# Performance work log

Measured on AMD Instinct MI355X. Metric: run time of the kernel, lower is better.

Reference implementation:

```python
import jax, jax.numpy as jnp
import numpy as np

B, M, N, D = 32, 10, 1000, 128
DEMAND_SCALER, SPEED_SCALER, PREF_SCALER = 40.0, 1.0, 1.0


def _pos_encoding(m, d, dtype):
    # standard sinusoidal PE over agent positions 0..m-1
    pos = jnp.arange(m, dtype=dtype)[:, None]
    div = jnp.exp(jnp.arange(0, d, 2, dtype=dtype) * (-jnp.log(jnp.asarray(10000.0, dtype)) / d))
    ang = pos * div  # (m, d/2)
    return jnp.stack([jnp.sin(ang), jnp.cos(ang)], axis=-1).reshape(m, d)  # even=sin, odd=cos


def setup_inputs() -> dict:
    key = jax.random.key(0)
    ks = jax.random.split(key, 14)
    return {
        "locs": jax.random.uniform(ks[0], (B, M + N, 2), jnp.float32),
        "capacity": jax.random.uniform(ks[1], (B, M), jnp.float32),
        "speed": jax.random.uniform(ks[2], (B, M), jnp.float32),
        "demand": jax.random.uniform(ks[3], (B, 1, M + N), jnp.float32),
        "agents_preference": jax.random.uniform(ks[4], (B, M, M + N), jnp.float32),
        "action_mask": jnp.ones((B, M, M + N), dtype=bool),
        "W_depot": jax.random.normal(ks[5], (D, 2), jnp.float32) * 0.1,
        "W_posproj": jax.random.normal(ks[6], (D, D), jnp.float32) * 0.05,
        "alpha": jnp.ones((1,), jnp.float32),
        "W_agents": jax.random.normal(ks[7], (D, 4), jnp.float32) * 0.1,
        "W_depot_agents": jax.random.normal(ks[8], (D, 2 * D), jnp.float32) * 0.05,
        "W_clients": jax.random.normal(ks[9], (D, 5), jnp.float32) * 0.1,
        "W_pref": jax.random.normal(ks[10], (D, 1), jnp.float32) * 0.1,
        "W_final": jax.random.normal(ks[11], (D, 3 * D), jnp.float32) * 0.05,
    }


def reference(locs, capacity, speed, demand, agents_preference, action_mask,
              W_depot, W_posproj, alpha, W_agents, W_depot_agents, W_clients,
              W_pref, W_final):
    m = action_mask.shape[-2]
    d = W_final.shape[0]
    depot_locs = locs[:, :m]            # (B, m, 2)
    agents_locs = locs[:, :m]
    clients_locs = locs[:, m:]          # (B, N, 2)

    # depot branch with positional encoding
    dep_emb = depot_locs @ W_depot.T                                   # (B, m, D)
    pe = _pos_encoding(m, d, dep_emb.dtype)                            # (m, D)
    depot_embedding = dep_emb + alpha[0] * (pe @ W_posproj.T)          # broadcast over B

    # agents branch
    agents_feats = jnp.concatenate(
        [agents_locs, capacity[..., None] / DEMAND_SCALER, speed[..., None] / SPEED_SCALER], axis=-1)
    agents_embedding = agents_feats @ W_agents.T                       # (B, m, D)
    depot_agents_embedding = jnp.concatenate(
        [depot_embedding, agents_embedding], axis=-1) @ W_depot_agents.T  # (B, m, D)

    # clients branch (with polar feats)
    demands = demand[:, 0, m:]                                         # (B, N)
    centered = clients_locs - depot_locs[:, 0:1]                       # (B, N, 2)
    dist = jnp.linalg.norm(centered, axis=-1, keepdims=True)
    angle = jnp.arctan2(centered[..., 1:], centered[..., :1])
    clients_feats = jnp.concatenate(
        [clients_locs, demands[..., None] / DEMAND_SCALER, dist, angle], axis=-1)
    clients_embedding = clients_feats @ W_clients.T                    # (B, N, D)

    nodes_embedding = jnp.concatenate([agents_embedding, clients_embedding], axis=1)  # (B, m+N, D)

    # fused final projection: Linear(3D, D) on cat([nodes, pref_embed, depot_agents])
    # == nodes @ Wn.T  +  pref_embed @ Wp.T  +  depot_agents @ Wd.T, broadcast over dims.
    # pref_embed = pref[..., None] * W_pref[:, 0]  (rank-1), so pref_embed @ Wp.T = pref[..., None] * (Wp @ W_pref[:, 0])
    Wn, Wp, Wd = W_final[:, :d], W_final[:, d:2 * d], W_final[:, 2 * d:]
    v_pref = Wp @ W_pref[:, 0]                                         # (D,)
    pref = agents_preference / PREF_SCALER                             # (B, m, m+N)
    combined_embedding = (
        (nodes_embedding @ Wn.T)[:, None, :, :]                        # (B, 1, m+N, D)
        + pref[..., None] * v_pref                                     # (B, m, m+N, D)
        + (depot_agents_embedding @ Wd.T)[:, :, None, :]               # (B, m, 1, D)
    )
    return nodes_embedding, combined_embedding
```

## Files before the change

kernel.cpp:

```cpp
#include <hip/hip_runtime.h>
#include <math.h>

#define BB 32
#define MM 10
#define NNODES 1010
#define DD 128
#define RPB 32
#define NG ((NNODES + RPB - 1) / RPB)

__global__ __launch_bounds__(512) void k_agents(
    const float* __restrict__ locs,
    const float* __restrict__ capacity,
    const float* __restrict__ speed,
    const float* __restrict__ W_depot,
    const float* __restrict__ W_posproj,
    const float* __restrict__ alpha,
    const float* __restrict__ W_agents,
    const float* __restrict__ W_da,
    const float* __restrict__ W_pref,
    const float* __restrict__ W_final,
    float* __restrict__ out_nodes,
    float* __restrict__ ws_daWd,
    float* __restrict__ ws_vpref)
{
    const int b = blockIdx.x / MM;
    const int m = blockIdx.x % MM;
    const int t = threadIdx.x;
    const int d = t & (DD - 1);
    const int q = t >> 7;

    __shared__ float pe_s[DD];
    __shared__ float dep_s[DD];
    __shared__ float ag_s[DD];
    __shared__ float da_s[DD];
    __shared__ float part[4][DD];

    if (q == 0) {
        const int i = d >> 1;
        const float div = expf((float)(2 * i) * (-logf(10000.0f) / (float)DD));
        const float ang = (float)m * div;
        pe_s[d] = (d & 1) ? cosf(ang) : sinf(ang);
    }
    __syncthreads();

    float pp = 0.0f;
    {
        const float4* wp  = (const float4*)(W_posproj + (size_t)d * DD + q * 32);
        const float4* pe4 = (const float4*)(pe_s + q * 32);
        #pragma unroll
        for (int k4 = 0; k4 < 8; ++k4) {
            const float4 w = wp[k4], p = pe4[k4];
            pp = fmaf(w.x, p.x, fmaf(w.y, p.y, fmaf(w.z, p.z, fmaf(w.w, p.w, pp))));
        }
    }
    part[q][d] = pp;
    __syncthreads();

    if (q == 0) {
        const float ppf = part[0][d] + part[1][d] + part[2][d] + part[3][d];
        const float lx = locs[((size_t)b * NNODES + m) * 2 + 0];
        const float ly = locs[((size_t)b * NNODES + m) * 2 + 1];
        const float dep = fmaf(lx, W_depot[d * 2 + 0],
                          fmaf(ly, W_depot[d * 2 + 1], alpha[0] * ppf));
        const float cap = capacity[b * MM + m] * (1.0f / 40.0f);
        const float spd = speed[b * MM + m];
        const float ag = fmaf(lx, W_agents[d * 4 + 0],
                         fmaf(ly, W_agents[d * 4 + 1],
                         fmaf(cap, W_agents[d * 4 + 2],
                              spd * W_agents[d * 4 + 3])));
        out_nodes[((size_t)b * NNODES + m) * DD + d] = ag;
        dep_s[d] = dep;
        ag_s[d] = ag;
    }
    __syncthreads();

    float da = 0.0f;
    {
        const float4* s4  = (const float4*)((q < 2) ? (dep_s + q * 64)
                                                    : (ag_s + (q - 2) * 64));
        const float4* wda = (const float4*)(W_da + (size_t)d * 2 * DD + q * 64);
        #pragma unroll
        for (int k4 = 0; k4 < 16; ++k4) {
            const float4 w = wda[k4], p = s4[k4];
            da = fmaf(w.x, p.x, fmaf(w.y, p.y, fmaf(w.z, p.z, fmaf(w.w, p.w, da))));
        }
    }
    part[q][d] = da;
    __syncthreads();
    if (q == 0) da_s[d] = part[0][d] + part[1][d] + part[2][d] + part[3][d];
    __syncthreads();

    float dw = 0.0f;
    {
        const float4* wfd = (const float4*)(W_final + (size_t)d * 3 * DD + 2 * DD + q * 32);
        const float4* s4  = (const float4*)(da_s + q * 32);
        #pragma unroll
        for (int k4 = 0; k4 < 8; ++k4) {
            const float4 w = wfd[k4], p = s4[k4];
            dw = fmaf(w.x, p.x, fmaf(w.y, p.y, fmaf(w.z, p.z, fmaf(w.w, p.w, dw))));
        }
    }
    part[q][d] = dw;
    __syncthreads();
    if (q == 0)
        ws_daWd[(b * MM + m) * DD + d] = part[0][d] + part[1][d] + part[2][d] + part[3][d];

    if (blockIdx.x == 0 && q == 3) {
        float vp = 0.0f;
        const float4* wfp = (const float4*)(W_final + (size_t)d * 3 * DD + DD);
        const float4* prf = (const float4*)W_pref;
        #pragma unroll
        for (int k4 = 0; k4 < DD / 4; ++k4) {
            const float4 w = wfp[k4], p = prf[k4];
            vp = fmaf(w.x, p.x, fmaf(w.y, p.y, fmaf(w.z, p.z, fmaf(w.w, p.w, vp))));
        }
        ws_vpref[d] = vp;
    }
}

__global__ __launch_bounds__(256) void k_main(
    const float* __restrict__ locs,
    const float* __restrict__ demand,
    const float* __restrict__ pref,
    const float* __restrict__ W_clients,
    const float* __restrict__ W_final,
    const float* __restrict__ ws_daWd,
    const float* __restrict__ ws_vpref,
    float* __restrict__ out_nodes,
    float* __restrict__ out_comb)
{
    const int g = blockIdx.x;
    const int b = blockIdx.y;
    const int t = threadIdx.x;
    const int n0 = g * RPB;

    __shared__ float rows[RPB][DD];
    __shared__ float feat[RPB][5];
    __shared__ float pref_s[MM][RPB];

    if (t < RPB) {
        const int node = n0 + t;
        if (node < NNODES && node >= MM) {
            const float cx = locs[((size_t)b * NNODES + node) * 2 + 0];
            const float cy = locs[((size_t)b * NNODES + node) * 2 + 1];
            const float d0x = locs[((size_t)b * NNODES + 0) * 2 + 0];
            const float d0y = locs[((size_t)b * NNODES + 0) * 2 + 1];
            const float dx = cx - d0x;
            const float dy = cy - d0y;
            feat[t][0] = cx;
            feat[t][1] = cy;
            feat[t][2] = demand[(size_t)b * NNODES + node] * (1.0f / 40.0f);
            feat[t][3] = sqrtf(fmaf(dx, dx, dy * dy));
            feat[t][4] = atan2f(dy, dx);
        }
    }
    for (int idx = t; idx < MM * RPB; idx += 256) {
        const int mm = idx >> 5;
        const int rr = idx & 31;
        const int node = n0 + rr;
        pref_s[mm][rr] = (node < NNODES)
            ? pref[(size_t)(b * MM + mm) * NNODES + node] : 0.0f;
    }
    __syncthreads();

    {
        const int d = t & (DD - 1);
        const int h = t >> 7;
        const float wc0 = W_clients[d * 5 + 0];
        const float wc1 = W_clients[d * 5 + 1];
        const float wc2 = W_clients[d * 5 + 2];
        const float wc3 = W_clients[d * 5 + 3];
        const float wc4 = W_clients[d * 5 + 4];
        #pragma unroll
        for (int i = 0; i < RPB / 2; ++i) {
            const int r = h * (RPB / 2) + i;
            const int node = n0 + r;
            float val = 0.0f;
            if (node < NNODES) {
                if (node < MM) {
                    val = out_nodes[((size_t)b * NNODES + node) * DD + d];
                } else {
                    val = fmaf(feat[r][0], wc0,
                          fmaf(feat[r][1], wc1,
                          fmaf(feat[r][2], wc2,
                          fmaf(feat[r][3], wc3,
                               feat[r][4] * wc4))));
                    out_nodes[((size_t)b * NNODES + node) * DD + d] = val;
                }
            }
            rows[r][d] = val;
        }
    }
    __syncthreads();

    const int c = t & 31;
    const int s = t >> 5;
    const int col = c * 4;
    float4 acc[4];
    #pragma unroll
    for (int j = 0; j < 4; ++j) acc[j] = make_float4(0.f, 0.f, 0.f, 0.f);

    {
        const float* w_base = W_final + (size_t)col * 3 * DD;
        #pragma unroll 4
        for (int k4 = 0; k4 < DD / 4; ++k4) {
            float4 w[4];
            #pragma unroll
            for (int i = 0; i < 4; ++i)
                w[i] = *(const float4*)(w_base + (size_t)i * 3 * DD + k4 * 4);
            #pragma unroll
            for (int j = 0; j < 4; ++j) {
                const float4 x = *(const float4*)&rows[s * 4 + j][k4 * 4];
                acc[j].x = fmaf(x.x, w[0].x, fmaf(x.y, w[0].y,
                           fmaf(x.z, w[0].z, fmaf(x.w, w[0].w, acc[j].x))));
                acc[j].y = fmaf(x.x, w[1].x, fmaf(x.y, w[1].y,
                           fmaf(x.z, w[1].z, fmaf(x.w, w[1].w, acc[j].y))));
                acc[j].z = fmaf(x.x, w[2].x, fmaf(x.y, w[2].y,
                           fmaf(x.z, w[2].z, fmaf(x.w, w[2].w, acc[j].z))));
                acc[j].w = fmaf(x.x, w[3].x, fmaf(x.y, w[3].y,
                           fmaf(x.z, w[3].z, fmaf(x.w, w[3].w, acc[j].w))));
            }
        }
    }

    const float4 vp = *(const float4*)(ws_vpref + col);
    float4 dawd[MM];
    #pragma unroll
    for (int mm = 0; mm < MM; ++mm)
        dawd[mm] = *(const float4*)(ws_daWd + (size_t)(b * MM + mm) * DD + col);

    #pragma unroll
    for (int mm = 0; mm < MM; ++mm) {
        #pragma unroll
        for (int j = 0; j < 4; ++j) {
            const int node = n0 + s * 4 + j;
            if (node >= NNODES) continue;
            const float pr = pref_s[mm][s * 4 + j];
            float4 o;
            o.x = fmaf(pr, vp.x, acc[j].x + dawd[mm].x);
            o.y = fmaf(pr, vp.y, acc[j].y + dawd[mm].y);
            o.z = fmaf(pr, vp.z, acc[j].z + dawd[mm].z);
            o.w = fmaf(pr, vp.w, acc[j].w + dawd[mm].w);
            *(float4*)(out_comb +
                ((size_t)(b * MM + mm) * NNODES + node) * DD + col) = o;
        }
    }
}

extern "C" void kernel_launch(void* const* d_in, const int* in_sizes, int n_in,
                              void* d_out, int out_size, void* d_ws, size_t ws_size,
                              hipStream_t stream) {
    const float* locs        = (const float*)d_in[0];
    const float* capacity    = (const float*)d_in[1];
    const float* speed       = (const float*)d_in[2];
    const float* demand      = (const float*)d_in[3];
    const float* agents_pref = (const float*)d_in[4];
    const float* W_depot     = (const float*)d_in[6];
    const float* W_posproj   = (const float*)d_in[7];
    const float* alpha       = (const float*)d_in[8];
    const float* W_agents    = (const float*)d_in[9];
    const float* W_da        = (const float*)d_in[10];
    const float* W_clients   = (const float*)d_in[11];
    const float* W_pref      = (const float*)d_in[12];
    const float* W_final     = (const float*)d_in[13];

    float* out_nodes = (float*)d_out;
    float* out_comb  = out_nodes + (size_t)BB * NNODES * DD;

    float* ws_daWd  = (float*)d_ws;
    float* ws_vpref = ws_daWd + BB * MM * DD;

    k_agents<<<dim3(BB * MM), 512, 0, stream>>>(
        locs, capacity, speed, W_depot, W_posproj, alpha, W_agents,
        W_da, W_pref, W_final, out_nodes, ws_daWd, ws_vpref);

    k_main<<<dim3(NG, BB), 256, 0, stream>>>(
        locs, demand, agents_pref, W_clients, W_final,
        ws_daWd, ws_vpref, out_nodes, out_comb);
}
```

Measured before the change: 268.5 us.

## Add prep kernel transposing weights and hoisting batch-independent PE projection

A new prep kernel transposes W_final's node and depot slices and W_da into k-major layouts in workspace. It also computes the per-agent positional-encoding projection and v_pref once, instead of redundantly in every (b,m) block. k_agents drops to 256 threads and reads the transposed weights with coalesced per-k loads, and k_main's GEMM reads W_n transposed so each float4 holds four output columns for one k. This adds an extra kernel launch and weight-transpose traffic each call in exchange for coalesced weight access and less redundant work.

```diff
diff --git a/kernel.cpp b/kernel.cpp
--- a/kernel.cpp
+++ b/kernel.cpp
@@ -6,62 +6,102 @@
 #define NNODES 1010
 #define DD 128
 #define RPB 32
-#define NG ((NNODES + RPB - 1) / RPB)
-
-__global__ __launch_bounds__(512) void k_agents(
+#define NG 32
+
+__global__ __launch_bounds__(256) void k_prep(
+    const float* __restrict__ W_posproj,
+    const float* __restrict__ W_da,
+    const float* __restrict__ W_pref,
+    const float* __restrict__ W_final,
+    float* __restrict__ wnT,
+    float* __restrict__ wdT,
+    float* __restrict__ wdaT,
+    float* __restrict__ vpref,
+    float* __restrict__ peproj)
+{
+    const int bk = blockIdx.x;
+    const int t = threadIdx.x;
+    const int d = t & (DD - 1);
+    const int h = t >> 7;
+
+    if (bk < 16) {
+        #pragma unroll
+        for (int kk = 0; kk < 4; ++kk) {
+            const int k = bk * 8 + h * 4 + kk;
+            wnT[k * DD + d] = W_final[(size_t)d * 384 + k];
+            wdT[k * DD + d] = W_final[(size_t)d * 384 + 256 + k];
+        }
+    } else if (bk < 32) {
+        #pragma unroll
+        for (int kk = 0; kk < 8; ++kk) {
+            const int k = (bk - 16) * 16 + h * 8 + kk;
+            wdaT[k * DD + d] = W_da[(size_t)d * 256 + k];
+        }
+    } else if (bk == 32) {
+        if (t < DD) {
+            float vp = 0.0f;
+            const float4* w = (const float4*)(W_final + (size_t)d * 384 + DD);
+            const float4* p = (const float4*)W_pref;
+            #pragma unroll
+            for (int k4 = 0; k4 < 32; ++k4) {
+                const float4 a = w[k4], b = p[k4];
+                vp = fmaf(a.x, b.x, fmaf(a.y, b.y, fmaf(a.z, b.z, fmaf(a.w, b.w, vp))));
+            }
+            vpref[d] = vp;
+        }
+    } else {
+        const int m = bk - 33;
+        __shared__ float pe_s[DD];
+        if (t < DD) {
+            const int i = d >> 1;
+            const float div = expf((float)(2 * i) * (-logf(10000.0f) / (float)DD));
+            const float ang = (float)m * div;
+            pe_s[d] = (d & 1) ? cosf(ang) : sinf(ang);
+        }
+        __syncthreads();
+        if (t < DD) {
+            float pp = 0.0f;
+            const float4* w = (const float4*)(W_posproj + (size_t)d * DD);
+            const float4* p = (const float4*)pe_s;
+            #pragma unroll
+            for (int k4 = 0; k4 < 32; ++k4) {
+                const float4 a = w[k4], b = p[k4];
+                pp = fmaf(a.x, b.x, fmaf(a.y, b.y, fmaf(a.z, b.z, fmaf(a.w, b.w, pp))));
+            }
+            peproj[m * DD + d] = pp;
+        }
+    }
+}
+
+__global__ __launch_bounds__(256) void k_agents(
     const float* __restrict__ locs,
     const float* __restrict__ capacity,
     const float* __restrict__ speed,
     const float* __restrict__ W_depot,
-    const float* __restrict__ W_posproj,
     const float* __restrict__ alpha,
     const float* __restrict__ W_agents,
-    const float* __restrict__ W_da,
-    const float* __restrict__ W_pref,
-    const float* __restrict__ W_final,
+    const float* __restrict__ wdaT,
+    const float* __restrict__ wdT,
+    const float* __restrict__ peproj,
     float* __restrict__ out_nodes,
-    float* __restrict__ ws_daWd,
-    float* __restrict__ ws_vpref)
+    float* __restrict__ ws_daWd)
 {
     const int b = blockIdx.x / MM;
     const int m = blockIdx.x % MM;
     const int t = threadIdx.x;
     const int d = t & (DD - 1);
-    const int q = t >> 7;
-
-    __shared__ float pe_s[DD];
-    __shared__ float dep_s[DD];
-    __shared__ float ag_s[DD];
+    const int h = t >> 7;
+
+    __shared__ float cat_s[2 * DD];
     __shared__ float da_s[DD];
-    __shared__ float part[4][DD];
-
-    if (q == 0) {
-        const int i = d >> 1;
-        const float div = expf((float)(2 * i) * (-logf(10000.0f) / (float)DD));
-        const float ang = (float)m * div;
-        pe_s[d] = (d & 1) ? cosf(ang) : sinf(ang);
-    }
-    __syncthreads();
-
-    float pp = 0.0f;
-    {
-        const float4* wp  = (const float4*)(W_posproj + (size_t)d * DD + q * 32);
-        const float4* pe4 = (const float4*)(pe_s + q * 32);
-        #pragma unroll
-        for (int k4 = 0; k4 < 8; ++k4) {
-            const float4 w = wp[k4], p = pe4[k4];
-            pp = fmaf(w.x, p.x, fmaf(w.y, p.y, fmaf(w.z, p.z, fmaf(w.w, p.w, pp))));
-        }
-    }
-    part[q][d] = pp;
-    __syncthreads();
-
-    if (q == 0) {
-        const float ppf = part[0][d] + part[1][d] + part[2][d] + part[3][d];
+    __shared__ float part[2][DD];
+
+    if (h == 0) {
         const float lx = locs[((size_t)b * NNODES + m) * 2 + 0];
         const float ly = locs[((size_t)b * NNODES + m) * 2 + 1];
         const float dep = fmaf(lx, W_depot[d * 2 + 0],
-                          fmaf(ly, W_depot[d * 2 + 1], alpha[0] * ppf));
+                          fmaf(ly, W_depot[d * 2 + 1],
+                               alpha[0] * peproj[m * DD + d]));
         const float cap = capacity[b * MM + m] * (1.0f / 40.0f);
         const float spd = speed[b * MM + m];
         const float ag = fmaf(lx, W_agents[d * 4 + 0],
@@ -69,53 +109,44 @@
                          fmaf(cap, W_agents[d * 4 + 2],
                               spd * W_agents[d * 4 + 3])));
         out_nodes[((size_t)b * NNODES + m) * DD + d] = ag;
-        dep_s[d] = dep;
-        ag_s[d] = ag;
-    }
-    __syncthreads();
-
-    float da = 0.0f;
+        cat_s[d] = dep;
+        cat_s[DD + d] = ag;
+    }
+    __syncthreads();
+
     {
-        const float4* s4  = (const float4*)((q < 2) ? (dep_s + q * 64)
-                                                    : (ag_s + (q - 2) * 64));
-        const float4* wda = (const float4*)(W_da + (size_t)d * 2 * DD + q * 64);
-        #pragma unroll
-        for (int k4 = 0; k4 < 16; ++k4) {
-            const float4 w = wda[k4], p = s4[k4];
-            da = fmaf(w.x, p.x, fmaf(w.y, p.y, fmaf(w.z, p.z, fmaf(w.w, p.w, da))));
-        }
-    }
-    part[q][d] = da;
-    __syncthreads();
-    if (q == 0) da_s[d] = part[0][d] + part[1][d] + part[2][d] + part[3][d];
-    __syncthreads();
-
-    float dw = 0.0f;
+        float a0 = 0.f, a1 = 0.f, a2 = 0.f, a3 = 0.f;
+        const float* wp = wdaT + (size_t)(h * DD) * DD + d;
+        const float* cp = cat_s + h * DD;
+        #pragma unroll 8
+        for (int k = 0; k < DD; k += 4) {
+            a0 = fmaf(cp[k + 0], wp[(size_t)(k + 0) * DD], a0);
+            a1 = fmaf(cp[k + 1], wp[(size_t)(k + 1) * DD], a1);
+            a2 = fmaf(cp[k + 2], wp[(size_t)(k + 2) * DD], a2);
+            a3 = fmaf(cp[k + 3], wp[(size_t)(k + 3) * DD], a3);
+        }
+        part[h][d] = (a0 + a1) + (a2 + a3);
+    }
+    __syncthreads();
+    if (h == 0) da_s[d] = part[0][d] + part[1][d];
+    __syncthreads();
+
     {
-        const float4* wfd = (const float4*)(W_final + (size_t)d * 3 * DD + 2 * DD + q * 32);
-        const float4* s4  = (const float4*)(da_s + q * 32);
-        #pragma unroll
-        for (int k4 = 0; k4 < 8; ++k4) {
-            const float4 w = wfd[k4], p = s4[k4];
-            dw = fmaf(w.x, p.x, fmaf(w.y, p.y, fmaf(w.z, p.z, fmaf(w.w, p.w, dw))));
-        }
-    }
-    part[q][d] = dw;
-    __syncthreads();
-    if (q == 0)
-        ws_daWd[(b * MM + m) * DD + d] = part[0][d] + part[1][d] + part[2][d] + part[3][d];
-
-    if (blockIdx.x == 0 && q == 3) {
-        float vp = 0.0f;
-        const float4* wfp = (const float4*)(W_final + (size_t)d * 3 * DD + DD);
-        const float4* prf = (const float4*)W_pref;
-        #pragma unroll
-        for (int k4 = 0; k4 < DD / 4; ++k4) {
-            const float4 w = wfp[k4], p = prf[k4];
-            vp = fmaf(w.x, p.x, fmaf(w.y, p.y, fmaf(w.z, p.z, fmaf(w.w, p.w, vp))));
-        }
-        ws_vpref[d] = vp;
-    }
+        float a0 = 0.f, a1 = 0.f, a2 = 0.f, a3 = 0.f;
+        const float* wp = wdT + (size_t)(h * 64) * DD + d;
+        const float* cp = da_s + h * 64;
+        #pragma unroll 4
+        for (int k = 0; k < 64; k += 4) {
+            a0 = fmaf(cp[k + 0], wp[(size_t)(k + 0) * DD], a0);
+            a1 = fmaf(cp[k + 1], wp[(size_t)(k + 1) * DD], a1);
+            a2 = fmaf(cp[k + 2], wp[(size_t)(k + 2) * DD], a2);
+            a3 = fmaf(cp[k + 3], wp[(size_t)(k + 3) * DD], a3);
+        }
+        part[h][d] = (a0 + a1) + (a2 + a3);
+    }
+    __syncthreads();
+    if (h == 0)
+        ws_daWd[(b * MM + m) * DD + d] = part[0][d] + part[1][d];
 }
 
 __global__ __launch_bounds__(256) void k_main(
@@ -123,7 +154,7 @@
     const float* __restrict__ demand,
     const float* __restrict__ pref,
     const float* __restrict__ W_clients,
-    const float* __restrict__ W_final,
+    const float* __restrict__ wnT,
     const float* __restrict__ ws_daWd,
     const float* __restrict__ ws_vpref,
     float* __restrict__ out_nodes,
@@ -201,24 +232,24 @@
     for (int j = 0; j < 4; ++j) acc[j] = make_float4(0.f, 0.f, 0.f, 0.f);
 
     {
-        const float* w_base = W_final + (size_t)col * 3 * DD;
-        #pragma unroll 4
+        const float* wt = wnT + col;
+        #pragma unroll 2
         for (int k4 = 0; k4 < DD / 4; ++k4) {
-            float4 w[4];
-            #pragma unroll
-            for (int i = 0; i < 4; ++i)
-                w[i] = *(const float4*)(w_base + (size_t)i * 3 * DD + k4 * 4);
+            const float4 w0 = *(const float4*)(wt + (size_t)(k4 * 4 + 0) * DD);
+            const float4 w1 = *(const float4*)(wt + (size_t)(k4 * 4 + 1) * DD);
+            const float4 w2 = *(const float4*)(wt + (size_t)(k4 * 4 + 2) * DD);
+            const float4 w3 = *(const float4*)(wt + (size_t)(k4 * 4 + 3) * DD);
             #pragma unroll
             for (int j = 0; j < 4; ++j) {
                 const float4 x = *(const float4*)&rows[s * 4 + j][k4 * 4];
-                acc[j].x = fmaf(x.x, w[0].x, fmaf(x.y, w[0].y,
-                           fmaf(x.z, w[0].z, fmaf(x.w, w[0].w, acc[j].x))));
-                acc[j].y = fmaf(x.x, w[1].x, fmaf(x.y, w[1].y,
-                           fmaf(x.z, w[1].z, fmaf(x.w, w[1].w, acc[j].y))));
-                acc[j].z = fmaf(x.x, w[2].x, fmaf(x.y, w[2].y,
-                           fmaf(x.z, w[2].z, fmaf(x.w, w[2].w, acc[j].z))));
-                acc[j].w = fmaf(x.x, w[3].x, fmaf(x.y, w[3].y,
-                           fmaf(x.z, w[3].z, fmaf(x.w, w[3].w, acc[j].w))));
+                acc[j].x = fmaf(x.x, w0.x, fmaf(x.y, w1.x,
+                           fmaf(x.z, w2.x, fmaf(x.w, w3.x, acc[j].x))));
+                acc[j].y = fmaf(x.x, w0.y, fmaf(x.y, w1.y,
+                           fmaf(x.z, w2.y, fmaf(x.w, w3.y, acc[j].y))));
+                acc[j].z = fmaf(x.x, w0.z, fmaf(x.y, w1.z,
+                           fmaf(x.z, w2.z, fmaf(x.w, w3.z, acc[j].z))));
+                acc[j].w = fmaf(x.x, w0.w, fmaf(x.y, w1.w,
+                           fmaf(x.z, w2.w, fmaf(x.w, w3.w, acc[j].w))));
             }
         }
     }
@@ -269,12 +300,20 @@
 
     float* ws_daWd  = (float*)d_ws;
     float* ws_vpref = ws_daWd + BB * MM * DD;
-
-    k_agents<<<dim3(BB * MM), 512, 0, stream>>>(
-        locs, capacity, speed, W_depot, W_posproj, alpha, W_agents,
-        W_da, W_pref, W_final, out_nodes, ws_daWd, ws_vpref);
+    float* ws_pepj  = ws_vpref + DD;
+    float* ws_wnT   = ws_pepj + MM * DD;
+    float* ws_wdT   = ws_wnT + DD * DD;
+    float* ws_wdaT  = ws_wdT + DD * DD;
+
+    k_prep<<<dim3(43), 256, 0, stream>>>(
+        W_posproj, W_da, W_pref, W_final,
+        ws_wnT, ws_wdT, ws_wdaT, ws_vpref, ws_pepj);
+
+    k_agents<<<dim3(BB * MM), 256, 0, stream>>>(
+        locs, capacity, speed, W_depot, alpha, W_agents,
+        ws_wdaT, ws_wdT, ws_pepj, out_nodes, ws_daWd);
 
     k_main<<<dim3(NG, BB), 256, 0, stream>>>(
-        locs, demand, agents_pref, W_clients, W_final,
+        locs, demand, agents_pref, W_clients, ws_wnT,
         ws_daWd, ws_vpref, out_nodes, out_comb);
 }
```

Result: faster. 234.3 us (-12.8%).

## Pre-transpose Wn, restructure agent kernel per batch, halve client row tile

Applied to the files above, without the earlier changes.

The front kernel now runs one block per batch and loops over the ten agents, keeping the W_posproj, W_depot_agents and W_final slices in registers and reducing with lane shuffles. Extra blocks in the same launch write a transposed copy of the node part of W_final and compute v_pref. The main kernel reads that transposed matrix so neighbouring threads load neighbouring columns, which should coalesce the weight loads. It also halves the rows per block to 16, doubling the grid for better occupancy. The cost is twice as many weight passes per output row, and a front kernel that handles agents one after another on only 32 blocks.

```diff
diff --git a/kernel.cpp b/kernel.cpp
--- a/kernel.cpp
+++ b/kernel.cpp
@@ -5,10 +5,10 @@
 #define MM 10
 #define NNODES 1010
 #define DD 128
-#define RPB 32
-#define NG ((NNODES + RPB - 1) / RPB)
-
-__global__ __launch_bounds__(512) void k_agents(
+#define RPB 16
+#define NG 64
+
+__global__ __launch_bounds__(512) void k_front(
     const float* __restrict__ locs,
     const float* __restrict__ capacity,
     const float* __restrict__ speed,
@@ -21,109 +21,139 @@
     const float* __restrict__ W_final,
     float* __restrict__ out_nodes,
     float* __restrict__ ws_daWd,
+    float* __restrict__ ws_wnT,
     float* __restrict__ ws_vpref)
 {
-    const int b = blockIdx.x / MM;
-    const int m = blockIdx.x % MM;
+    const int bk = blockIdx.x;
     const int t = threadIdx.x;
-    const int d = t & (DD - 1);
-    const int q = t >> 7;
-
-    __shared__ float pe_s[DD];
-    __shared__ float dep_s[DD];
-    __shared__ float ag_s[DD];
-    __shared__ float da_s[DD];
-    __shared__ float part[4][DD];
-
-    if (q == 0) {
-        const int i = d >> 1;
-        const float div = expf((float)(2 * i) * (-logf(10000.0f) / (float)DD));
-        const float ang = (float)m * div;
-        pe_s[d] = (d & 1) ? cosf(ang) : sinf(ang);
-    }
-    __syncthreads();
-
-    float pp = 0.0f;
-    {
-        const float4* wp  = (const float4*)(W_posproj + (size_t)d * DD + q * 32);
-        const float4* pe4 = (const float4*)(pe_s + q * 32);
+
+    if (bk < BB) {
+        const int b = bk;
+        const int d = t >> 2;
+        const int q = t & 3;
+
+        __shared__ float pe_s[MM][DD];
+        __shared__ float cat_s[2 * DD];
+        __shared__ float da_s[DD];
+
+        for (int idx = t; idx < MM * DD; idx += 512) {
+            const int m = idx >> 7;
+            const int k = idx & (DD - 1);
+            const int i = k >> 1;
+            const float div = expf((float)(2 * i) * (-logf(10000.0f) / (float)DD));
+            const float ang = (float)m * div;
+            pe_s[m][k] = (k & 1) ? cosf(ang) : sinf(ang);
+        }
+
+        float4 wpp[8], wfd[8], wda[16];
+        {
+            const float4* p = (const float4*)(W_posproj + (size_t)d * DD + q * 32);
+            #pragma unroll
+            for (int i = 0; i < 8; ++i) wpp[i] = p[i];
+        }
+        {
+            const float4* p = (const float4*)(W_da + (size_t)d * 256 + q * 64);
+            #pragma unroll
+            for (int i = 0; i < 16; ++i) wda[i] = p[i];
+        }
+        {
+            const float4* p = (const float4*)(W_final + (size_t)d * 384 + 256 + q * 32);
+            #pragma unroll
+            for (int i = 0; i < 8; ++i) wfd[i] = p[i];
+        }
+        const float wd0 = W_depot[d * 2 + 0], wd1 = W_depot[d * 2 + 1];
+        const float wa0 = W_agents[d * 4 + 0], wa1 = W_agents[d * 4 + 1];
+        const float wa2 = W_agents[d * 4 + 2], wa3 = W_agents[d * 4 + 3];
+        const float al = alpha[0];
+        __syncthreads();
+
+        for (int m = 0; m < MM; ++m) {
+            float pp = 0.0f;
+            {
+                const float4* pe4 = (const float4*)(&pe_s[m][q * 32]);
+                #pragma unroll
+                for (int i = 0; i < 8; ++i) {
+                    const float4 w = wpp[i], x = pe4[i];
+                    pp = fmaf(w.x, x.x, fmaf(w.y, x.y, fmaf(w.z, x.z, fmaf(w.w, x.w, pp))));
+                }
+            }
+            pp += __shfl_xor(pp, 1, 4);
+            pp += __shfl_xor(pp, 2, 4);
+
+            if (q == 0) {
+                const float lx = locs[((size_t)b * NNODES + m) * 2 + 0];
+                const float ly = locs[((size_t)b * NNODES + m) * 2 + 1];
+                const float dep = fmaf(lx, wd0, fmaf(ly, wd1, al * pp));
+                const float cap = capacity[b * MM + m] * (1.0f / 40.0f);
+                const float spd = speed[b * MM + m];
+                const float ag = fmaf(lx, wa0, fmaf(ly, wa1,
+                                 fmaf(cap, wa2, spd * wa3)));
+                out_nodes[((size_t)b * NNODES + m) * DD + d] = ag;
+                cat_s[d] = dep;
+                cat_s[DD + d] = ag;
+            }
+            __syncthreads();
+
+            float da = 0.0f;
+            {
+                const float4* c4 = (const float4*)(cat_s + q * 64);
+                #pragma unroll
+                for (int i = 0; i < 16; ++i) {
+                    const float4 w = wda[i], x = c4[i];
+                    da = fmaf(w.x, x.x, fmaf(w.y, x.y, fmaf(w.z, x.z, fmaf(w.w, x.w, da))));
+                }
+            }
+            da += __shfl_xor(da, 1, 4);
+            da += __shfl_xor(da, 2, 4);
+            if (q == 0) da_s[d] = da;
+            __syncthreads();
+
+            float dw = 0.0f;
+            {
+                const float4* c4 = (const float4*)(da_s + q * 32);
+                #pragma unroll
+                for (int i = 0; i < 8; ++i) {
+                    const float4 w = wfd[i], x = c4[i];
+                    dw = fmaf(w.x, x.x, fmaf(w.y, x.y, fmaf(w.z, x.z, fmaf(w.w, x.w, dw))));
+                }
+            }
+            dw += __shfl_xor(dw, 1, 4);
+            dw += __shfl_xor(dw, 2, 4);
+            if (q == 0)
+                ws_daWd[(b * MM + m) * DD + d] = dw;
+            __syncthreads();
+        }
+    } else if (bk < 48) {
+        const int d = t & (DD - 1);
+        const int j = t >> 7;
+        const int k0 = (bk - 32) * 8;
         #pragma unroll
-        for (int k4 = 0; k4 < 8; ++k4) {
-            const float4 w = wp[k4], p = pe4[k4];
-            pp = fmaf(w.x, p.x, fmaf(w.y, p.y, fmaf(w.z, p.z, fmaf(w.w, p.w, pp))));
-        }
-    }
-    part[q][d] = pp;
-    __syncthreads();
-
-    if (q == 0) {
-        const float ppf = part[0][d] + part[1][d] + part[2][d] + part[3][d];
-        const float lx = locs[((size_t)b * NNODES + m) * 2 + 0];
-        const float ly = locs[((size_t)b * NNODES + m) * 2 + 1];
-        const float dep = fmaf(lx, W_depot[d * 2 + 0],
-                          fmaf(ly, W_depot[d * 2 + 1], alpha[0] * ppf));
-        const float cap = capacity[b * MM + m] * (1.0f / 40.0f);
-        const float spd = speed[b * MM + m];
-        const float ag = fmaf(lx, W_agents[d * 4 + 0],
-                         fmaf(ly, W_agents[d * 4 + 1],
-                         fmaf(cap, W_agents[d * 4 + 2],
-                              spd * W_agents[d * 4 + 3])));
-        out_nodes[((size_t)b * NNODES + m) * DD + d] = ag;
-        dep_s[d] = dep;
-        ag_s[d] = ag;
-    }
-    __syncthreads();
-
-    float da = 0.0f;
-    {
-        const float4* s4  = (const float4*)((q < 2) ? (dep_s + q * 64)
-                                                    : (ag_s + (q - 2) * 64));
-        const float4* wda = (const float4*)(W_da + (size_t)d * 2 * DD + q * 64);
-        #pragma unroll
-        for (int k4 = 0; k4 < 16; ++k4) {
-            const float4 w = wda[k4], p = s4[k4];
-            da = fmaf(w.x, p.x, fmaf(w.y, p.y, fmaf(w.z, p.z, fmaf(w.w, p.w, da))));
-        }
-    }
-    part[q][d] = da;
-    __syncthreads();
-    if (q == 0) da_s[d] = part[0][d] + part[1][d] + part[2][d] + part[3][d];
-    __syncthreads();
-
-    float dw = 0.0f;
-    {
-        const float4* wfd = (const float4*)(W_final + (size_t)d * 3 * DD + 2 * DD + q * 32);
-        const float4* s4  = (const float4*)(da_s + q * 32);
-        #pragma unroll
-        for (int k4 = 0; k4 < 8; ++k4) {
-            const float4 w = wfd[k4], p = s4[k4];
-            dw = fmaf(w.x, p.x, fmaf(w.y, p.y, fmaf(w.z, p.z, fmaf(w.w, p.w, dw))));
-        }
-    }
-    part[q][d] = dw;
-    __syncthreads();
-    if (q == 0)
-        ws_daWd[(b * MM + m) * DD + d] = part[0][d] + part[1][d] + part[2][d] + part[3][d];
-
-    if (blockIdx.x == 0 && q == 3) {
-        float vp = 0.0f;
-        const float4* wfp = (const float4*)(W_final + (size_t)d * 3 * DD + DD);
-        const float4* prf = (const float4*)W_pref;
-        #pragma unroll
-        for (int k4 = 0; k4 < DD / 4; ++k4) {
-            const float4 w = wfp[k4], p = prf[k4];
-            vp = fmaf(w.x, p.x, fmaf(w.y, p.y, fmaf(w.z, p.z, fmaf(w.w, p.w, vp))));
-        }
-        ws_vpref[d] = vp;
+        for (int l = 0; l < 2; ++l) {
+            const int k = k0 + j * 2 + l;
+            ws_wnT[k * DD + d] = W_final[(size_t)d * 384 + k];
+        }
+    } else {
+        if (t < DD) {
+            const int d = t;
+            float vp = 0.0f;
+            const float4* w = (const float4*)(W_final + (size_t)d * 384 + DD);
+            const float4* p = (const float4*)W_pref;
+            #pragma unroll
+            for (int k4 = 0; k4 < 32; ++k4) {
+                const float4 a = w[k4], bb = p[k4];
+                vp = fmaf(a.x, bb.x, fmaf(a.y, bb.y, fmaf(a.z, bb.z, fmaf(a.w, bb.w, vp))));
+            }
+            ws_vpref[d] = vp;
+        }
     }
 }
 
-__global__ __launch_bounds__(256) void k_main(
+__global__ __launch_bounds__(256) void k_back(
     const float* __restrict__ locs,
     const float* __restrict__ demand,
     const float* __restrict__ pref,
     const float* __restrict__ W_clients,
-    const float* __restrict__ W_final,
+    const float* __restrict__ wnT,
     const float* __restrict__ ws_daWd,
     const float* __restrict__ ws_vpref,
     float* __restrict__ out_nodes,
@@ -154,9 +184,9 @@
             feat[t][4] = atan2f(dy, dx);
         }
     }
-    for (int idx = t; idx < MM * RPB; idx += 256) {
-        const int mm = idx >> 5;
-        const int rr = idx & 31;
+    if (t < MM * RPB) {
+        const int mm = t >> 4;
+        const int rr = t & 15;
         const int node = n0 + rr;
         pref_s[mm][rr] = (node < NNODES)
             ? pref[(size_t)(b * MM + mm) * NNODES + node] : 0.0f;
@@ -191,51 +221,51 @@
             rows[r][d] = val;
         }
     }
-    __syncthreads();
 
     const int c = t & 31;
     const int s = t >> 5;
     const int col = c * 4;
-    float4 acc[4];
-    #pragma unroll
-    for (int j = 0; j < 4; ++j) acc[j] = make_float4(0.f, 0.f, 0.f, 0.f);
-
-    {
-        const float* w_base = W_final + (size_t)col * 3 * DD;
-        #pragma unroll 4
-        for (int k4 = 0; k4 < DD / 4; ++k4) {
-            float4 w[4];
-            #pragma unroll
-            for (int i = 0; i < 4; ++i)
-                w[i] = *(const float4*)(w_base + (size_t)i * 3 * DD + k4 * 4);
-            #pragma unroll
-            for (int j = 0; j < 4; ++j) {
-                const float4 x = *(const float4*)&rows[s * 4 + j][k4 * 4];
-                acc[j].x = fmaf(x.x, w[0].x, fmaf(x.y, w[0].y,
-                           fmaf(x.z, w[0].z, fmaf(x.w, w[0].w, acc[j].x))));
-                acc[j].y = fmaf(x.x, w[1].x, fmaf(x.y, w[1].y,
-                           fmaf(x.z, w[1].z, fmaf(x.w, w[1].w, acc[j].y))));
-                acc[j].z = fmaf(x.x, w[2].x, fmaf(x.y, w[2].y,
-                           fmaf(x.z, w[2].z, fmaf(x.w, w[2].w, acc[j].z))));
-                acc[j].w = fmaf(x.x, w[3].x, fmaf(x.y, w[3].y,
-                           fmaf(x.z, w[3].z, fmaf(x.w, w[3].w, acc[j].w))));
-            }
-        }
-    }
-
     const float4 vp = *(const float4*)(ws_vpref + col);
     float4 dawd[MM];
     #pragma unroll
     for (int mm = 0; mm < MM; ++mm)
         dawd[mm] = *(const float4*)(ws_daWd + (size_t)(b * MM + mm) * DD + col);
 
+    __syncthreads();
+
+    float4 acc[2];
+    acc[0] = make_float4(0.f, 0.f, 0.f, 0.f);
+    acc[1] = make_float4(0.f, 0.f, 0.f, 0.f);
+    {
+        const float* wt = wnT + col;
+        #pragma unroll 4
+        for (int k4 = 0; k4 < DD / 4; ++k4) {
+            const float4 w0 = *(const float4*)(wt + (size_t)(k4 * 4 + 0) * DD);
+            const float4 w1 = *(const float4*)(wt + (size_t)(k4 * 4 + 1) * DD);
+            const float4 w2 = *(const float4*)(wt + (size_t)(k4 * 4 + 2) * DD);
+            const float4 w3 = *(const float4*)(wt + (size_t)(k4 * 4 + 3) * DD);
+            #pragma unroll
+            for (int j = 0; j < 2; ++j) {
+                const float4 x = *(const float4*)&rows[s * 2 + j][k4 * 4];
+                acc[j].x = fmaf(x.x, w0.x, fmaf(x.y, w1.x,
+                           fmaf(x.z, w2.x, fmaf(x.w, w3.x, acc[j].x))));
+                acc[j].y = fmaf(x.x, w0.y, fmaf(x.y, w1.y,
+                           fmaf(x.z, w2.y, fmaf(x.w, w3.y, acc[j].y))));
+                acc[j].z = fmaf(x.x, w0.z, fmaf(x.y, w1.z,
+                           fmaf(x.z, w2.z, fmaf(x.w, w3.z, acc[j].z))));
+                acc[j].w = fmaf(x.x, w0.w, fmaf(x.y, w1.w,
+                           fmaf(x.z, w2.w, fmaf(x.w, w3.w, acc[j].w))));
+            }
+        }
+    }
+
     #pragma unroll
     for (int mm = 0; mm < MM; ++mm) {
         #pragma unroll
-        for (int j = 0; j < 4; ++j) {
-            const int node = n0 + s * 4 + j;
+        for (int j = 0; j < 2; ++j) {
+            const int node = n0 + s * 2 + j;
             if (node >= NNODES) continue;
-            const float pr = pref_s[mm][s * 4 + j];
+            const float pr = pref_s[mm][s * 2 + j];
             float4 o;
             o.x = fmaf(pr, vp.x, acc[j].x + dawd[mm].x);
             o.y = fmaf(pr, vp.y, acc[j].y + dawd[mm].y);
@@ -269,12 +299,13 @@
 
     float* ws_daWd  = (float*)d_ws;
     float* ws_vpref = ws_daWd + BB * MM * DD;
-
-    k_agents<<<dim3(BB * MM), 512, 0, stream>>>(
+    float* ws_wnT   = ws_vpref + DD;
+
+    k_front<<<dim3(49), 512, 0, stream>>>(
         locs, capacity, speed, W_depot, W_posproj, alpha, W_agents,
-        W_da, W_pref, W_final, out_nodes, ws_daWd, ws_vpref);
-
-    k_main<<<dim3(NG, BB), 256, 0, stream>>>(
-        locs, demand, agents_pref, W_clients, W_final,
+        W_da, W_pref, W_final, out_nodes, ws_daWd, ws_wnT, ws_vpref);
+
+    k_back<<<dim3(NG, BB), 256, 0, stream>>>(
+        locs, demand, agents_pref, W_clients, ws_wnT,
         ws_daWd, ws_vpref, out_nodes, out_comb);
 }
```

New measurement: 256.6 us. 4.4% less time.
